# Performance work log

Hardware: AMD Instinct MI355X
Metric: run time of the kernel (lower is better)

The kernel has to match this reference:

```python
import jax, jax.numpy as jnp
import numpy as np

D, H, DH, DFF, K = 512, 8, 64, 2048, 31
B, T = 8, 1024


def _ln(x, g, b):
    m = x.mean(-1, keepdims=True)
    v = ((x - m) ** 2).mean(-1, keepdims=True)
    return (x - m) / jnp.sqrt(v + 1e-5) * g + b


def _silu(x):
    return x * jax.nn.sigmoid(x)


def _pe(t, d):
    i = jnp.arange(t, dtype=jnp.float32)[:, None]
    j = jnp.arange(0, d, 2, dtype=jnp.float32)
    ang = i * (1.0 / (10000.0 ** (j / d)))
    pe = jnp.zeros((t, d), jnp.float32)
    pe = pe.at[:, 0::2].set(jnp.sin(ang))
    pe = pe.at[:, 1::2].set(jnp.cos(ang))
    return pe


def setup_inputs() -> dict:
    key = jax.random.key(0)
    ks = iter(jax.random.split(key, 40))
    s = 0.02
    d = {
        'x': jax.random.normal(next(ks), (B, T, D), jnp.float32),
        # FF module 1
        'ff1_ln_g': jnp.ones((D,), jnp.float32), 'ff1_ln_b': jnp.zeros((D,), jnp.float32),
        'ff1_w1': jax.random.normal(next(ks), (D, DFF), jnp.float32) * s,
        'ff1_b1': jnp.zeros((DFF,), jnp.float32),
        'ff1_w2': jax.random.normal(next(ks), (DFF, D), jnp.float32) * s,
        'ff1_b2': jnp.zeros((D,), jnp.float32),
        # MHSA
        'mha_ln_g': jnp.ones((D,), jnp.float32), 'mha_ln_b': jnp.zeros((D,), jnp.float32),
        'wq': jax.random.normal(next(ks), (H, D, DH), jnp.float32) * s,
        'bq': jnp.zeros((H, DH), jnp.float32),
        'wk': jax.random.normal(next(ks), (H, D, DH), jnp.float32) * s,
        'bk': jnp.zeros((H, DH), jnp.float32),
        'wv': jax.random.normal(next(ks), (H, D, DH), jnp.float32) * s,
        'bv': jnp.zeros((H, DH), jnp.float32),
        'wo': jax.random.normal(next(ks), (D, D), jnp.float32) * s,
        'bo': jnp.zeros((D,), jnp.float32),
        # Conv module
        'cv_ln_g': jnp.ones((D,), jnp.float32), 'cv_ln_b': jnp.zeros((D,), jnp.float32),
        'cv_w1': jax.random.normal(next(ks), (2 * D, D), jnp.float32) * s,
        'cv_b1': jnp.zeros((2 * D,), jnp.float32),
        'cv_wd': jax.random.normal(next(ks), (D, D, K), jnp.float32) * s,
        'cv_bn_g': jnp.ones((D,), jnp.float32), 'cv_bn_b': jnp.zeros((D,), jnp.float32),
        'cv_w2': jax.random.normal(next(ks), (D, D), jnp.float32) * s,
        'cv_b2': jnp.zeros((D,), jnp.float32),
        # FF module 2
        'ff2_ln_g': jnp.ones((D,), jnp.float32), 'ff2_ln_b': jnp.zeros((D,), jnp.float32),
        'ff2_w1': jax.random.normal(next(ks), (D, DFF), jnp.float32) * s,
        'ff2_b1': jnp.zeros((DFF,), jnp.float32),
        'ff2_w2': jax.random.normal(next(ks), (DFF, D), jnp.float32) * s,
        'ff2_b2': jnp.zeros((D,), jnp.float32),
        # final layer norm
        'fin_g': jnp.ones((D,), jnp.float32), 'fin_b': jnp.zeros((D,), jnp.float32),
    }
    return d


def _block(x, p):
    def ffn(x, g, b, w1, b1, w2, b2):
        y = _silu(_ln(x, g, b) @ w1 + b1) @ w2 + b2
        return x + y  # FeedForwardModule internal residual

    # x = x + 0.5 * ff_1(x)
    x = x + 0.5 * ffn(x, p['ff1_ln_g'], p['ff1_ln_b'], p['ff1_w1'], p['ff1_b1'], p['ff1_w2'], p['ff1_b2'])

    # MHSA module (with its own internal residual), then block residual
    y = _ln(x, p['mha_ln_g'], p['mha_ln_b']) + _pe(x.shape[1], x.shape[2])
    q = jnp.einsum('btd,hde->bhte', y, p['wq']) + p['bq'][None, :, None, :]
    k = jnp.einsum('btd,hde->bhte', y, p['wk']) + p['bk'][None, :, None, :]
    v = jnp.einsum('btd,hde->bhte', y, p['wv']) + p['bv'][None, :, None, :]
    scores = jnp.einsum('bhtd,bhsd->bhts', q, k) * (1.0 / np.sqrt(DH))
    attn = jax.nn.softmax(scores, axis=-1)
    o = jnp.einsum('bhts,bhsd->bhtd', attn, v)
    # faithful to original: raw view [B,H,T,dh] -> [B,T,H*dh] (no transpose)
    o = o.reshape(x.shape[0], x.shape[1], H * DH)
    o = o @ p['wo'] + p['bo']
    x = x + (x + o)

    # Convolution module (internal residual), then block residual
    y = _ln(x, p['cv_ln_g'], p['cv_ln_b']).swapaxes(1, 2)  # [B,D,T]
    y = jnp.einsum('ed,bdt->bet', p['cv_w1'], y) + p['cv_b1'][None, :, None]
    a, g = jnp.split(y, 2, axis=1)
    y = a * jax.nn.sigmoid(g)  # GLU over channel dim
    y = jax.lax.conv_general_dilated(y, p['cv_wd'], (1,), [(K // 2, K // 2)],
                                     dimension_numbers=('NCH', 'OIH', 'NCH'))
    # BatchNorm1d in training mode: batch stats over (batch, time), biased variance
    m = y.mean((0, 2), keepdims=True)
    var = ((y - m) ** 2).mean((0, 2), keepdims=True)
    y = (y - m) / jnp.sqrt(var + 1e-5) * p['cv_bn_g'][None, :, None] + p['cv_bn_b'][None, :, None]
    y = _silu(y)
    y = jnp.einsum('ed,bdt->bet', p['cv_w2'], y) + p['cv_b2'][None, :, None]
    y = y.swapaxes(1, 2)
    x = x + (x + y)

    # x = x + 0.5 * ff_2(x)
    x = x + 0.5 * ffn(x, p['ff2_ln_g'], p['ff2_ln_b'], p['ff2_w1'], p['ff2_b1'], p['ff2_w2'], p['ff2_b2'])

    return _ln(x, p['fin_g'], p['fin_b'])


def reference(x, ff1_ln_g, ff1_ln_b, ff1_w1, ff1_b1, ff1_w2, ff1_b2,
              mha_ln_g, mha_ln_b, wq, bq, wk, bk, wv, bv, wo, bo,
              cv_ln_g, cv_ln_b, cv_w1, cv_b1, cv_wd, cv_bn_g, cv_bn_b, cv_w2, cv_b2,
              ff2_ln_g, ff2_ln_b, ff2_w1, ff2_b1, ff2_w2, ff2_b2,
              fin_g, fin_b):
    p = dict(ff1_ln_g=ff1_ln_g, ff1_ln_b=ff1_ln_b, ff1_w1=ff1_w1, ff1_b1=ff1_b1,
             ff1_w2=ff1_w2, ff1_b2=ff1_b2, mha_ln_g=mha_ln_g, mha_ln_b=mha_ln_b,
             wq=wq, bq=bq, wk=wk, bk=bk, wv=wv, bv=bv, wo=wo, bo=bo,
             cv_ln_g=cv_ln_g, cv_ln_b=cv_ln_b, cv_w1=cv_w1, cv_b1=cv_b1, cv_wd=cv_wd,
             cv_bn_g=cv_bn_g, cv_bn_b=cv_bn_b, cv_w2=cv_w2, cv_b2=cv_b2,
             ff2_ln_g=ff2_ln_g, ff2_ln_b=ff2_ln_b, ff2_w1=ff2_w1, ff2_b1=ff2_b1,
             ff2_w2=ff2_w2, ff2_b2=ff2_b2, fin_g=fin_g, fin_b=fin_b)
    return _block(x, p)
```

## Files before the change

kernel.cpp:

```cpp
#include <hip/hip_runtime.h>


typedef __attribute__((ext_vector_type(4))) float f32x4;
typedef __attribute__((ext_vector_type(8))) short short8;
typedef __attribute__((ext_vector_type(4))) short s16x4;

__device__ __forceinline__ float bfs2f(short s) {
  unsigned u = ((unsigned)(unsigned short)s) << 16;
  float f; __builtin_memcpy(&f, &u, 4); return f;
}
__device__ __forceinline__ short f2bfs(float f) {
  unsigned u; __builtin_memcpy(&u, &f, 4);
  u = (u + 0x7FFFu + ((u >> 16) & 1u)) >> 16;
  return (short)u;
}
__device__ __forceinline__ float sigmoidf_(float x) { return 1.f / (1.f + __expf(-x)); }

#define GLOADLDS(gsrc, ldst) \
  __builtin_amdgcn_global_load_lds((__attribute__((address_space(1))) void*)(gsrc), \
                                   (__attribute__((address_space(3))) void*)(ldst), 16, 0, 0)

#define VMCNT_ASM(n) asm volatile("s_waitcnt vmcnt(" #n ")" ::: "memory")
template<int N> __device__ __forceinline__ void vmcnt_wait() {
  if      constexpr (N == 0)  VMCNT_ASM(0);
  else if constexpr (N == 2)  VMCNT_ASM(2);
  else if constexpr (N == 3)  VMCNT_ASM(3);
  else if constexpr (N == 4)  VMCNT_ASM(4);
  else if constexpr (N == 6)  VMCNT_ASM(6);
  else if constexpr (N == 8)  VMCNT_ASM(8);
  else                        VMCNT_ASM(0);
}
#define MEMFENCE asm volatile("" ::: "memory")

enum { EPI_SILU = 0, EPI_F32BIAS = 1, EPI_RES = 2, EPI_QKV = 3, EPI_F32 = 6 };

template<int BM, int BN, int WM, int WN, int EPI>
__global__ __launch_bounds__(256) void gemm_bt(
    const short* __restrict__ A, int lda, long zAh, long zAl,
    const short* __restrict__ BT, int ldbt, long zBh, long zBl,
    int K, int Kdec,
    void* C, int ldc, long zCh, long zCl, int zdiv,
    const float* bias, const float* bias2, const float* bias3,
    const float* resid, float alpha, float beta)
{
  constexpr int FM = BM / (WM * 16), FN = BN / (WN * 16);
  constexpr int AIT = (BM * 4) / 256, BIT = (BN * 4) / 256;
  constexpr int L = AIT + BIT;
  __shared__ short sA[3][BM * 32];
  __shared__ short sB[3][BN * 32];
  const int tid = threadIdx.x;
  const int zmask = (1 << zdiv) - 1;
  const int zhi = (int)(blockIdx.z >> zdiv);
  const int zlo = (int)(blockIdx.z & zmask);
  A  += (long)zhi * zAh + (long)zlo * zAl;
  BT += (long)zhi * zBh + (long)zlo * zBl;
  char* cbase = (char*)C + (long)zhi * zCh + (long)zlo * zCl;
  const int m0 = blockIdx.x * BM, n0 = blockIdx.y * BN;
  const int Keff = K - (zlo == zmask ? Kdec : 0);

  auto stage = [&](int buf, int k0) {
#pragma unroll
    for (int it = 0; it < AIT; ++it) {
      int idx = it * 256 + tid;
      GLOADLDS(A + (long)(m0 + (idx >> 2)) * lda + k0 + (idx & 3) * 8, &sA[buf][idx * 8]);
    }
#pragma unroll
    for (int it = 0; it < BIT; ++it) {
      int idx = it * 256 + tid;
      GLOADLDS(BT + (long)(n0 + (idx >> 2)) * ldbt + k0 + (idx & 3) * 8, &sB[buf][idx * 8]);
    }
  };

  f32x4 acc[FM][FN];
#pragma unroll
  for (int i = 0; i < FM; ++i) {
#pragma unroll
    for (int j = 0; j < FN; ++j) acc[i][j] = (f32x4){0.f, 0.f, 0.f, 0.f};
  }
  const int lane = tid & 63, wid = tid >> 6;
  const int wm = wid / WN, wn = wid % WN;
  const int lr = lane & 15, kg = lane >> 4;
  const int aRow = wm * (BM / WM), bRow = wn * (BN / WN);

  const int nt = Keff >> 5;
  stage(0, 0);
  stage(1, 32);
  vmcnt_wait<L>();
  __builtin_amdgcn_s_barrier();

  int cur = 0, sbuf = 2;
  for (int t = 0; t < nt; ++t) {
    const bool st = (t + 2 < nt);
    if (st) stage(sbuf, (t + 2) * 32);
    short8 af[FM], bfr[FN];
#pragma unroll
    for (int mi = 0; mi < FM; ++mi)
      af[mi] = *(const short8*)&sA[cur][(aRow + mi * 16 + lr) * 32 + kg * 8];
#pragma unroll
    for (int ni = 0; ni < FN; ++ni)
      bfr[ni] = *(const short8*)&sB[cur][(bRow + ni * 16 + lr) * 32 + kg * 8];
#pragma unroll
    for (int mi = 0; mi < FM; ++mi) {
#pragma unroll
      for (int ni = 0; ni < FN; ++ni)
        acc[mi][ni] = __builtin_amdgcn_mfma_f32_16x16x32_bf16(af[mi], bfr[ni], acc[mi][ni], 0, 0, 0);
    }
    if (st) vmcnt_wait<L>(); else vmcnt_wait<0>();
    __builtin_amdgcn_s_barrier();
    cur = (cur == 2) ? 0 : cur + 1;
    sbuf = (sbuf == 2) ? 0 : sbuf + 1;
  }

  const int baseRow = m0 + aRow, baseCol = n0 + bRow;
#pragma unroll
  for (int mi = 0; mi < FM; ++mi) {
#pragma unroll
    for (int ni = 0; ni < FN; ++ni) {
      const int col = baseCol + ni * 16 + lr;
#pragma unroll
      for (int r = 0; r < 4; ++r) {
        const int row = baseRow + mi * 16 + kg * 4 + r;
        float v = acc[mi][ni][r];
        if (EPI == EPI_SILU) {
          v += bias[col];
          v = v * sigmoidf_(v);
          ((short*)cbase)[(long)row * ldc + col] = f2bfs(v);
        } else if (EPI == EPI_F32BIAS) {
          v += bias[col];
          ((float*)cbase)[(long)row * ldc + col] = v;
        } else if (EPI == EPI_RES) {
          v += bias[col];
          float rv = resid[(long)row * ldc + col];
          ((float*)cbase)[(long)row * ldc + col] = alpha * rv + beta * v;
        } else if (EPI == EPI_QKV) {
          if (col < 512)       v = (v + bias[col]) * 0.125f;
          else if (col < 1024) v += bias2[col - 512];
          else                 v += bias3[col - 1024];
          ((short*)cbase)[(long)row * ldc + col] = f2bfs(v);
        } else if (EPI == EPI_F32) {
          ((float*)cbase)[(long)row * ldc + col] = v;
        }
      }
    }
  }
}

__global__ __launch_bounds__(256) void conv_tap(
    const short* __restrict__ glu,
    const short* __restrict__ wdP,
    short* __restrict__ parts)
{
  __shared__ short sA[2][144 * 32];
  const int tid = threadIdx.x;
  const int bid = blockIdx.x;
  const int cc = bid & 7, j = bid >> 3;
  const int y = cc >> 1, kg = cc & 1;
  const int x = j & 7, b = j >> 3;
  const int m0 = x * 128, n0 = y * 128;
  const short* Arow0 = glu + ((long)b * 1056 + m0 + 1 + kg * 16) * 512;
  short* cbase = parts + (long)kg * (8192L * 512) + (long)b * (1024L * 512);

  const int lane = tid & 63, wid = tid >> 6;
  const int wm = wid >> 1, wn = wid & 1;
  const int lr = lane & 15, kgr = lane >> 4;
  const int aRow = wm * 64, bRow = wn * 64;

  const short* Bp = wdP + (long)((n0 + bRow) >> 4) * (512L * 512)
                  + (long)(kg * 256) * 512 + lane * 8;
  const long NSTR = 512L * 512;

  auto stageA = [&](int buf, int ib) {
#pragma unroll
    for (int it = 0; it < 3; ++it) {
      int idx = it * 256 + tid;
      if (idx < 576) {
        GLOADLDS(Arow0 + (long)(idx >> 2) * 512 + ib * 32 + (idx & 3) * 8,
                 &sA[buf][idx * 8]);
      }
    }
  };

  f32x4 acc[4][4];
#pragma unroll
  for (int i = 0; i < 4; ++i) {
#pragma unroll
    for (int jj = 0; jj < 4; ++jj) acc[i][jj] = (f32x4){0.f, 0.f, 0.f, 0.f};
  }
  short8 b0[4], b1[4];

  stageA(0, 0);
  MEMFENCE;
#pragma unroll
  for (int ni = 0; ni < 4; ++ni)
    b0[ni] = *(const short8*)(Bp + ni * NSTR);
  MEMFENCE;
  vmcnt_wait<4>();
  __builtin_amdgcn_s_barrier();

  int cur = 0;
  for (int ib = 0; ib < 16; ++ib) {
    if (ib + 1 < 16) stageA(cur ^ 1, ib + 1);
    MEMFENCE;
#pragma unroll
    for (int kk = 0; kk < 16; ++kk) {
      const long noff = (kk + 1 < 16) ? (long)((kk + 1) * 16 + ib) * 512
                                      : (long)(ib + 1) * 512;
      if ((kk & 1) == 0) {
#pragma unroll
        for (int ni = 0; ni < 4; ++ni)
          b1[ni] = *(const short8*)(Bp + noff + ni * NSTR);
      } else {
#pragma unroll
        for (int ni = 0; ni < 4; ++ni)
          b0[ni] = *(const short8*)(Bp + noff + ni * NSTR);
      }
      short8 af[4];
#pragma unroll
      for (int mi = 0; mi < 4; ++mi)
        af[mi] = *(const short8*)&sA[cur][(kk + aRow + mi * 16 + lr) * 32 + kgr * 8];
      __builtin_amdgcn_s_setprio(1);
      if ((kk & 1) == 0) {
#pragma unroll
        for (int mi = 0; mi < 4; ++mi) {
#pragma unroll
          for (int ni = 0; ni < 4; ++ni)
            acc[mi][ni] = __builtin_amdgcn_mfma_f32_16x16x32_bf16(af[mi], b0[ni], acc[mi][ni], 0, 0, 0);
        }
      } else {
#pragma unroll
        for (int mi = 0; mi < 4; ++mi) {
#pragma unroll
          for (int ni = 0; ni < 4; ++ni)
            acc[mi][ni] = __builtin_amdgcn_mfma_f32_16x16x32_bf16(af[mi], b1[ni], acc[mi][ni], 0, 0, 0);
        }
      }
      __builtin_amdgcn_s_setprio(0);
    }
    vmcnt_wait<4>();
    __builtin_amdgcn_s_barrier();
    cur ^= 1;
  }
  vmcnt_wait<0>();

  const int baseRow = m0 + aRow, baseCol = n0 + bRow;
#pragma unroll
  for (int mi = 0; mi < 4; ++mi) {
#pragma unroll
    for (int ni = 0; ni < 4; ++ni) {
      const int col = baseCol + ni * 16 + lr;
#pragma unroll
      for (int r = 0; r < 4; ++r) {
        const int row = baseRow + mi * 16 + kgr * 4 + r;
        cbase[(long)row * 512 + col] = f2bfs(acc[mi][ni][r]);
      }
    }
  }
}

__global__ __launch_bounds__(256) void flash_attn(
    const short* __restrict__ qkv,
    const short* __restrict__ vt,
    short* __restrict__ out)
{
  __shared__ short sQ[64 * 64];
  __shared__ short sK[64 * 64];
  __shared__ short sV[64 * 64];
  __shared__ short sP[4][16 * 64];
  const int tid = threadIdx.x;
  const int lane = tid & 63, w = tid >> 6;
  const int lr = lane & 15, kg = lane >> 4;
  const int bh = (int)blockIdx.z;
  const int b = bh >> 3, h = bh & 7;
  const int q0 = blockIdx.x * 64;
  const short* qbase = qkv + (long)b * 1024 * 1536 + h * 64;
  const short* kbase = qbase + 512;
  const short* vtb = vt + (long)bh * 65536;

#pragma unroll
  for (int it = 0; it < 2; ++it) {
    int idx = it * 256 + tid;
    int row = idx >> 3, c = (idx & 7) ^ (row & 7);
    GLOADLDS(qbase + (long)(q0 + row) * 1536 + c * 8, &sQ[idx * 8]);
  }
  __syncthreads();
  short8 bq[2];
#pragma unroll
  for (int ks = 0; ks < 2; ++ks)
    bq[ks] = *(const short8*)&sQ[(w * 16 + lr) * 64 + ((ks * 4 + kg) ^ (lr & 7)) * 8];

  f32x4 po[4];
#pragma unroll
  for (int mi = 0; mi < 4; ++mi) po[mi] = (f32x4){0.f, 0.f, 0.f, 0.f};
  float m = -3.0e38f, l = 0.f;

  for (int s0 = 0; s0 < 1024; s0 += 64) {
#pragma unroll
    for (int it = 0; it < 2; ++it) {
      int idx = it * 256 + tid;
      int row = idx >> 3, c = (idx & 7) ^ (row & 7);
      GLOADLDS(kbase + (long)(s0 + row) * 1536 + c * 8, &sK[idx * 8]);
    }
#pragma unroll
    for (int it = 0; it < 2; ++it) {
      int idx = it * 256 + tid;
      int row = idx >> 3, c = (idx & 7) ^ (row & 7);
      GLOADLDS(vtb + (long)row * 1024 + s0 + c * 8, &sV[idx * 8]);
    }
    __syncthreads();

    f32x4 as[4];
#pragma unroll
    for (int mi = 0; mi < 4; ++mi) as[mi] = (f32x4){0.f, 0.f, 0.f, 0.f};
    __builtin_amdgcn_s_setprio(1);
#pragma unroll
    for (int ks = 0; ks < 2; ++ks) {
#pragma unroll
      for (int mi = 0; mi < 4; ++mi) {
        short8 ak = *(const short8*)&sK[(mi * 16 + lr) * 64 + ((ks * 4 + kg) ^ (lr & 7)) * 8];
        as[mi] = __builtin_amdgcn_mfma_f32_16x16x32_bf16(ak, bq[ks], as[mi], 0, 0, 0);
      }
    }
    __builtin_amdgcn_s_setprio(0);

    float rmax = as[0][0];
#pragma unroll
    for (int mi = 0; mi < 4; ++mi) {
#pragma unroll
      for (int r = 0; r < 4; ++r) rmax = fmaxf(rmax, as[mi][r]);
    }
    rmax = fmaxf(rmax, __shfl_xor(rmax, 16));
    rmax = fmaxf(rmax, __shfl_xor(rmax, 32));
    const float mn = fmaxf(m, rmax);
    const float sc = __expf(m - mn);
    float p[4][4];
    float rsum = 0.f;
#pragma unroll
    for (int mi = 0; mi < 4; ++mi) {
#pragma unroll
      for (int r = 0; r < 4; ++r) { p[mi][r] = __expf(as[mi][r] - mn); rsum += p[mi][r]; }
    }
    rsum += __shfl_xor(rsum, 16);
    rsum += __shfl_xor(rsum, 32);
    l = l * sc + rsum;
    m = mn;
#pragma unroll
    for (int mi = 0; mi < 4; ++mi) {
#pragma unroll
      for (int r = 0; r < 4; ++r) po[mi][r] *= sc;
    }
#pragma unroll
    for (int mi = 0; mi < 4; ++mi) {
      s16x4 pk;
#pragma unroll
      for (int r = 0; r < 4; ++r) pk[r] = f2bfs(p[mi][r]);
      *(s16x4*)&sP[w][lr * 64 + ((mi ^ (lr & 3)) * 16 + kg * 4)] = pk;
    }
    __builtin_amdgcn_s_setprio(1);
#pragma unroll
    for (int ks = 0; ks < 2; ++ks) {
      short8 bp = *(const short8*)&sP[w][lr * 64 + (((ks * 2 + (kg >> 1)) ^ (lr & 3)) * 16 + (kg & 1) * 8)];
#pragma unroll
      for (int mi = 0; mi < 4; ++mi) {
        short8 av = *(const short8*)&sV[(mi * 16 + lr) * 64 + ((ks * 4 + kg) ^ (lr & 7)) * 8];
        po[mi] = __builtin_amdgcn_mfma_f32_16x16x32_bf16(av, bp, po[mi], 0, 0, 0);
      }
    }
    __builtin_amdgcn_s_setprio(0);
    __syncthreads();
  }

  const float inv = 1.f / l;
  const int t2 = q0 + w * 16 + lr;
  const int n = h * 1024 + t2;
  short* ob = out + ((long)b * 1024 + (n >> 3)) * 512 + (n & 7) * 64;
#pragma unroll
  for (int mi = 0; mi < 4; ++mi) {
    s16x4 o;
#pragma unroll
    for (int r = 0; r < 4; ++r) o[r] = f2bfs(po[mi][r] * inv);
    *(s16x4*)&ob[mi * 16 + kg * 4] = o;
  }
}

__global__ __launch_bounds__(256) void reduce_bn(
    const short* __restrict__ parts, long pstride,
    short* __restrict__ z, float* stats)
{
  const int r0 = blockIdx.x * 16;
  const int c = threadIdx.x * 2;
  float s0 = 0.f, s1 = 0.f, q0 = 0.f, q1 = 0.f;
#pragma unroll 4
  for (int r = 0; r < 16; ++r) {
    const long idx = (long)(r0 + r) * 512 + c;
    int p0 = *(const int*)&parts[idx];
    int p1 = *(const int*)&parts[idx + pstride];
    float a0 = bfs2f((short)(p0 & 0xffff)) + bfs2f((short)(p1 & 0xffff));
    float a1 = bfs2f((short)(p0 >> 16)) + bfs2f((short)(p1 >> 16));
    int zo = ((int)(unsigned short)f2bfs(a0)) | (((int)(unsigned short)f2bfs(a1)) << 16);
    *(int*)&z[idx] = zo;
    s0 += a0; s1 += a1; q0 += a0 * a0; q1 += a1 * a1;
  }
  atomicAdd(&stats[c], s0);
  atomicAdd(&stats[c + 1], s1);
  atomicAdd(&stats[512 + c], q0);
  atomicAdd(&stats[512 + c + 1], q1);
}

template<int ADDPE, int OUTF32>
__global__ __launch_bounds__(256) void ln_rows(
    const float* __restrict__ X, const float* __restrict__ g, const float* __restrict__ b,
    const float* __restrict__ pe, void* __restrict__ Y)
{
  const int row = blockIdx.x * 4 + (threadIdx.x >> 6);
  const int lane = threadIdx.x & 63;
  const int c0 = lane * 8;
  const float* src = X + (long)row * 512 + c0;
  f32x4 a = *(const f32x4*)src, c = *(const f32x4*)(src + 4);
  float x[8] = {a[0], a[1], a[2], a[3], c[0], c[1], c[2], c[3]};
  float s = 0.f, q = 0.f;
#pragma unroll
  for (int j = 0; j < 8; ++j) { s += x[j]; q += x[j] * x[j]; }
#pragma unroll
  for (int off = 32; off > 0; off >>= 1) { s += __shfl_xor(s, off); q += __shfl_xor(q, off); }
  const float mean = s * (1.f / 512.f);
  const float var = q * (1.f / 512.f) - mean * mean;
  const float rstd = rsqrtf(var + 1e-5f);
  f32x4 g0 = *(const f32x4*)(g + c0), g1 = *(const f32x4*)(g + c0 + 4);
  f32x4 b0 = *(const f32x4*)(b + c0), b1 = *(const f32x4*)(b + c0 + 4);
  float gg[8] = {g0[0], g0[1], g0[2], g0[3], g1[0], g1[1], g1[2], g1[3]};
  float bb[8] = {b0[0], b0[1], b0[2], b0[3], b1[0], b1[1], b1[2], b1[3]};
  float y[8];
#pragma unroll
  for (int j = 0; j < 8; ++j) {
    y[j] = (x[j] - mean) * rstd * gg[j] + bb[j];
    if (ADDPE) y[j] += pe[(long)(row & 1023) * 512 + c0 + j];
  }
  if (OUTF32) {
    float* dst = (float*)Y + (long)row * 512 + c0;
    *(f32x4*)dst = (f32x4){y[0], y[1], y[2], y[3]};
    *(f32x4*)(dst + 4) = (f32x4){y[4], y[5], y[6], y[7]};
  } else {
    short8 o;
#pragma unroll
    for (int j = 0; j < 8; ++j) o[j] = f2bfs(y[j]);
    *(short8*)((short*)Y + (long)row * 512 + c0) = o;
  }
}

template<int INF32>
__global__ __launch_bounds__(256) void transpose64(
    const void* __restrict__ in_, int ldin, short* __restrict__ out, int ldout,
    int ctiles, int zshift, long zh_in, long zl_in, long z_out)
{
  __shared__ short t[64][72];
  const int z = blockIdx.z;
  const long inoff = (long)(z >> zshift) * zh_in + (long)(z & ((1 << zshift) - 1)) * zl_in;
  const int tr = blockIdx.x / ctiles, tc = blockIdx.x % ctiles;
  short* dst = out + (long)z * z_out + (long)(tc * 64) * ldout + tr * 64;
  const int tid = threadIdx.x;
#pragma unroll
  for (int p = 0; p < 2; ++p) {
    int idx = p * 256 + tid;
    int r = idx >> 3, c8 = (idx & 7) * 8;
    if (INF32) {
      const float* src = (const float*)in_ + inoff + (long)(tr * 64 + r) * ldin + tc * 64 + c8;
      f32x4 v0 = *(const f32x4*)src, v1 = *(const f32x4*)(src + 4);
#pragma unroll
      for (int j = 0; j < 4; ++j) { t[r][c8 + j] = f2bfs(v0[j]); t[r][c8 + 4 + j] = f2bfs(v1[j]); }
    } else {
      const short* src = (const short*)in_ + inoff + (long)(tr * 64 + r) * ldin + tc * 64 + c8;
      short8 v = *(const short8*)src;
#pragma unroll
      for (int j = 0; j < 8; ++j) t[r][c8 + j] = v[j];
    }
  }
  __syncthreads();
#pragma unroll
  for (int p = 0; p < 2; ++p) {
    int idx = p * 256 + tid;
    int c = idx >> 3, r8 = (idx & 7) * 8;
    short8 v;
#pragma unroll
    for (int j = 0; j < 8; ++j) v[j] = t[r8 + j][c];
    *(short8*)(dst + (long)c * ldout + r8) = v;
  }
}

__global__ __launch_bounds__(256) void wd_pack(const float* __restrict__ wd, short* __restrict__ wdP)
{
  const int gid = blockIdx.x * 256 + threadIdx.x;
  const int e = gid >> 9, i = gid & 511;
  const float* src = wd + ((long)e * 512 + i) * 31;
  const long rowtile = (long)(e >> 4) * (512L * 512);
  const int inner = ((i >> 3) & 3) * 128 + (e & 15) * 8 + (i & 7);
#pragma unroll
  for (int KK = 0; KK < 31; ++KK)
    wdP[rowtile + (long)(KK * 16 + (i >> 5)) * 512 + inner] = f2bfs(src[KK]);
  wdP[rowtile + (long)(31 * 16 + (i >> 5)) * 512 + inner] = 0;
}

__global__ __launch_bounds__(256) void pe_init(float* __restrict__ pe)
{
  const int gid = blockIdx.x * 256 + threadIdx.x;
  const int t = gid >> 8, p = gid & 255;
  const float freq = __expf(-(float)p * (9.210340371976184f / 256.f));
  const float ang = (float)t * freq;
  pe[(long)t * 512 + 2 * p]     = sinf(ang);
  pe[(long)t * 512 + 2 * p + 1] = cosf(ang);
}

__global__ __launch_bounds__(256) void glu_kernel(const float* __restrict__ y1, short* __restrict__ gp)
{
  const int gid = blockIdx.x * 256 + threadIdx.x;
  const int row = gid >> 7;
  const int ci = (gid & 127) * 4;
  const float* base = y1 + (long)row * 1024;
  f32x4 a = *(const f32x4*)(base + ci);
  f32x4 g = *(const f32x4*)(base + 512 + ci);
  const int b = row >> 10, t = row & 1023;
  s16x4 o;
#pragma unroll
  for (int j = 0; j < 4; ++j) o[j] = f2bfs(a[j] * sigmoidf_(g[j]));
  *(s16x4*)(gp + ((long)b * 1056 + 16 + t) * 512 + ci) = o;
}

__global__ void bn_stats(float* stats, const float* __restrict__ bn_g, const float* __restrict__ bn_b)
{
  const int c = blockIdx.x * 256 + threadIdx.x;
  if (c < 512) {
    float mean = stats[c] * (1.f / 8192.f);
    float var = stats[512 + c] * (1.f / 8192.f) - mean * mean;
    float sc = bn_g[c] * rsqrtf(var + 1e-5f);
    stats[1024 + c] = sc;
    stats[1536 + c] = bn_b[c] - mean * sc;
  }
}

__global__ __launch_bounds__(256) void bn_silu(const short* __restrict__ z, const float* __restrict__ stats,
                                               short* __restrict__ out)
{
  const long base = ((long)blockIdx.x * 256 + threadIdx.x) * 8;
  const int c0 = (int)(base & 511);
  short8 v = *(const short8*)(z + base);
  short8 o;
#pragma unroll
  for (int j = 0; j < 8; ++j) {
    const int c = c0 + j;
    float y = bfs2f(v[j]) * stats[1024 + c] + stats[1536 + c];
    o[j] = f2bfs(y * sigmoidf_(y));
  }
  *(short8*)(out + base) = o;
}

__global__ __launch_bounds__(256) void cast_bf16(const float* __restrict__ in, short* __restrict__ out, long n)
{
  for (long i = (long)blockIdx.x * 256 + threadIdx.x; i < n; i += (long)gridDim.x * 256)
    out[i] = f2bfs(in[i]);
}

extern "C" void kernel_launch(void* const* d_in, const int* in_sizes, int n_in,
                              void* d_out, int out_size, void* d_ws, size_t ws_size,
                              hipStream_t stream)
{
  (void)in_sizes; (void)n_in; (void)out_size; (void)ws_size;
  const float* x_in   = (const float*)d_in[0];
  const float* ff1_g  = (const float*)d_in[1];
  const float* ff1_bb = (const float*)d_in[2];
  const float* ff1_w1 = (const float*)d_in[3];
  const float* ff1_b1 = (const float*)d_in[4];
  const float* ff1_w2 = (const float*)d_in[5];
  const float* ff1_b2 = (const float*)d_in[6];
  const float* mha_g  = (const float*)d_in[7];
  const float* mha_b  = (const float*)d_in[8];
  const float* wq     = (const float*)d_in[9];
  const float* bq     = (const float*)d_in[10];
  const float* wk     = (const float*)d_in[11];
  const float* bk     = (const float*)d_in[12];
  const float* wv     = (const float*)d_in[13];
  const float* bv     = (const float*)d_in[14];
  const float* wo     = (const float*)d_in[15];
  const float* bo     = (const float*)d_in[16];
  const float* cv_g   = (const float*)d_in[17];
  const float* cv_b   = (const float*)d_in[18];
  const float* cv_w1  = (const float*)d_in[19];
  const float* cv_b1  = (const float*)d_in[20];
  const float* cv_wd  = (const float*)d_in[21];
  const float* bn_g   = (const float*)d_in[22];
  const float* bn_b   = (const float*)d_in[23];
  const float* cv_w2  = (const float*)d_in[24];
  const float* cv_b2  = (const float*)d_in[25];
  const float* ff2_g  = (const float*)d_in[26];
  const float* ff2_b  = (const float*)d_in[27];
  const float* ff2_w1 = (const float*)d_in[28];
  const float* ff2_b1 = (const float*)d_in[29];
  const float* ff2_w2 = (const float*)d_in[30];
  const float* ff2_b2 = (const float*)d_in[31];
  const float* fin_g  = (const float*)d_in[32];
  const float* fin_b  = (const float*)d_in[33];

  size_t off = 0;
  char* wsb = (char*)d_ws;
  auto take = [&](size_t n) { char* p = wsb + off; off += (n + 255) & ~(size_t)255; return p; };
  short* ff1w1T = (short*)take(2048L * 512 * 2);
  short* ff1w2T = (short*)take(512L * 2048 * 2);
  short* qkvT   = (short*)take(1536L * 512 * 2);
  short* woT    = (short*)take(512L * 512 * 2);
  short* cw1b   = (short*)take(1024L * 512 * 2);
  short* cw2b   = (short*)take(512L * 512 * 2);
  short* wdP    = (short*)take(32L * 512 * 512 * 2);
  short* ff2w1T = (short*)take(2048L * 512 * 2);
  short* ff2w2T = (short*)take(512L * 2048 * 2);
  float* xcur   = (float*)take(8192L * 512 * 4);
  char*  Ra     = take(8192L * 2048 * 2);
  short* Rb     = (short*)take(8192L * 512 * 2);
  short* Rg     = (short*)take((8L * 1056 + 2) * 512 * 2);
  short* parts  = (short*)take(2L * 8192 * 512 * 2);
  short* vt     = (short*)take(64L * 64 * 1024 * 2);
  float* pe     = (float*)take(1024L * 512 * 4);
  float* stats  = (float*)take(2048L * 4);

  short* hid = (short*)Ra;
  short* qkv = (short*)Ra;
  float* y1  = (float*)Ra;

  transpose64<1><<<dim3(256, 1, 1), 256, 0, stream>>>(ff1_w1, 2048, ff1w1T, 512, 32, 0, 0, 0, 0);
  transpose64<1><<<dim3(256, 1, 1), 256, 0, stream>>>(ff1_w2, 512, ff1w2T, 2048, 8, 0, 0, 0, 0);
  transpose64<1><<<dim3(8, 1, 8), 256, 0, stream>>>(wq, 64, qkvT, 512, 1, 0, 32768, 0, 32768);
  transpose64<1><<<dim3(8, 1, 8), 256, 0, stream>>>(wk, 64, qkvT + 512 * 512, 512, 1, 0, 32768, 0, 32768);
  transpose64<1><<<dim3(8, 1, 8), 256, 0, stream>>>(wv, 64, qkvT + 1024 * 512, 512, 1, 0, 32768, 0, 32768);
  transpose64<1><<<dim3(64, 1, 1), 256, 0, stream>>>(wo, 512, woT, 512, 8, 0, 0, 0, 0);
  transpose64<1><<<dim3(256, 1, 1), 256, 0, stream>>>(ff2_w1, 2048, ff2w1T, 512, 32, 0, 0, 0, 0);
  transpose64<1><<<dim3(256, 1, 1), 256, 0, stream>>>(ff2_w2, 512, ff2w2T, 2048, 8, 0, 0, 0, 0);
  wd_pack<<<1024, 256, 0, stream>>>(cv_wd, wdP);
  pe_init<<<1024, 256, 0, stream>>>(pe);
  cast_bf16<<<2048, 256, 0, stream>>>(cv_w1, cw1b, 524288L);
  cast_bf16<<<1024, 256, 0, stream>>>(cv_w2, cw2b, 262144L);

  ln_rows<0, 0><<<2048, 256, 0, stream>>>(x_in, ff1_g, ff1_bb, nullptr, Rb);
  gemm_bt<128, 128, 2, 2, EPI_SILU><<<dim3(64, 16, 1), 256, 0, stream>>>(
      Rb, 512, 0, 0, ff1w1T, 512, 0, 0, 512, 0,
      hid, 2048, 0, 0, 0, ff1_b1, nullptr, nullptr, nullptr, 0.f, 0.f);
  gemm_bt<64, 64, 2, 2, EPI_RES><<<dim3(128, 8, 1), 256, 0, stream>>>(
      hid, 2048, 0, 0, ff1w2T, 2048, 0, 0, 2048, 0,
      xcur, 512, 0, 0, 0, ff1_b2, nullptr, nullptr, x_in, 1.5f, 0.5f);

  ln_rows<1, 0><<<2048, 256, 0, stream>>>(xcur, mha_g, mha_b, pe, Rb);
  gemm_bt<128, 128, 2, 2, EPI_QKV><<<dim3(64, 12, 1), 256, 0, stream>>>(
      Rb, 512, 0, 0, qkvT, 512, 0, 0, 512, 0,
      qkv, 1536, 0, 0, 0, bq, bk, bv, nullptr, 0.f, 0.f);
  transpose64<0><<<dim3(16, 1, 64), 256, 0, stream>>>(qkv + 1024, 1536, vt, 1024, 1, 3,
                                                      1024L * 1536, 64, 65536);
  flash_attn<<<dim3(16, 1, 64), 256, 0, stream>>>(qkv, vt, Rb);
  gemm_bt<64, 64, 2, 2, EPI_RES><<<dim3(128, 8, 1), 256, 0, stream>>>(
      Rb, 512, 0, 0, woT, 512, 0, 0, 512, 0,
      xcur, 512, 0, 0, 0, bo, nullptr, nullptr, xcur, 2.f, 1.f);

  ln_rows<0, 0><<<2048, 256, 0, stream>>>(xcur, cv_g, cv_b, nullptr, Rb);
  gemm_bt<128, 128, 2, 2, EPI_F32BIAS><<<dim3(64, 8, 1), 256, 0, stream>>>(
      Rb, 512, 0, 0, cw1b, 512, 0, 0, 512, 0,
      y1, 1024, 0, 0, 0, cv_b1, nullptr, nullptr, nullptr, 0.f, 0.f);
  (void)hipMemsetAsync(Rg, 0, (8L * 1056 + 2) * 512 * 2, stream);
  glu_kernel<<<4096, 256, 0, stream>>>(y1, Rg);
  (void)hipMemsetAsync(stats, 0, 1024 * sizeof(float), stream);
  conv_tap<<<512, 256, 0, stream>>>(Rg, wdP, parts);
  reduce_bn<<<512, 256, 0, stream>>>(parts, 8192L * 512, Rb, stats);
  bn_stats<<<2, 256, 0, stream>>>(stats, bn_g, bn_b);
  bn_silu<<<2048, 256, 0, stream>>>(Rb, stats, (short*)Rg);
  gemm_bt<64, 64, 2, 2, EPI_RES><<<dim3(128, 8, 1), 256, 0, stream>>>(
      (short*)Rg, 512, 0, 0, cw2b, 512, 0, 0, 512, 0,
      xcur, 512, 0, 0, 0, cv_b2, nullptr, nullptr, xcur, 2.f, 1.f);

  ln_rows<0, 0><<<2048, 256, 0, stream>>>(xcur, ff2_g, ff2_b, nullptr, Rb);
  gemm_bt<128, 128, 2, 2, EPI_SILU><<<dim3(64, 16, 1), 256, 0, stream>>>(
      Rb, 512, 0, 0, ff2w1T, 512, 0, 0, 512, 0,
      hid, 2048, 0, 0, 0, ff2_b1, nullptr, nullptr, nullptr, 0.f, 0.f);
  gemm_bt<64, 64, 2, 2, EPI_RES><<<dim3(128, 8, 1), 256, 0, stream>>>(
      hid, 2048, 0, 0, ff2w2T, 2048, 0, 0, 2048, 0,
      xcur, 512, 0, 0, 0, ff2_b2, nullptr, nullptr, xcur, 1.5f, 0.5f);

  ln_rows<0, 1><<<2048, 256, 0, stream>>>(xcur, fin_g, fin_b, nullptr, (float*)d_out);
}
```

Measured before the change: 508.0 us.

## Store conv pointwise output in bf16, zero only halo rows, raise MFMA priority

The first conv pointwise GEMM now writes bf16 instead of fp32, which halves the y1 write and the GLU read traffic, and the GLU kernel converts on load. The full memset of the padded GLU buffer is replaced by a small kernel that zeroes only the halo rows the GLU kernel does not write. The GEMM main loop also wraps its MFMA block in s_setprio 1/0 so these waves get scheduling priority. The extra bf16 rounding of the pre-GLU activations adds a small accuracy risk.

```diff
diff --git a/kernel.cpp b/kernel.cpp
--- a/kernel.cpp
+++ b/kernel.cpp
@@ -32,7 +32,7 @@
 }
 #define MEMFENCE asm volatile("" ::: "memory")
 
-enum { EPI_SILU = 0, EPI_F32BIAS = 1, EPI_RES = 2, EPI_QKV = 3, EPI_F32 = 6 };
+enum { EPI_SILU = 0, EPI_BBIAS = 1, EPI_RES = 2, EPI_QKV = 3, EPI_F32 = 6 };
 
 template<int BM, int BN, int WM, int WN, int EPI>
 __global__ __launch_bounds__(256) void gemm_bt(
@@ -99,12 +99,14 @@
 #pragma unroll
     for (int ni = 0; ni < FN; ++ni)
       bfr[ni] = *(const short8*)&sB[cur][(bRow + ni * 16 + lr) * 32 + kg * 8];
+    __builtin_amdgcn_s_setprio(1);
 #pragma unroll
     for (int mi = 0; mi < FM; ++mi) {
 #pragma unroll
       for (int ni = 0; ni < FN; ++ni)
         acc[mi][ni] = __builtin_amdgcn_mfma_f32_16x16x32_bf16(af[mi], bfr[ni], acc[mi][ni], 0, 0, 0);
     }
+    __builtin_amdgcn_s_setprio(0);
     if (st) vmcnt_wait<L>(); else vmcnt_wait<0>();
     __builtin_amdgcn_s_barrier();
     cur = (cur == 2) ? 0 : cur + 1;
@@ -125,9 +127,9 @@
           v += bias[col];
           v = v * sigmoidf_(v);
           ((short*)cbase)[(long)row * ldc + col] = f2bfs(v);
-        } else if (EPI == EPI_F32BIAS) {
+        } else if (EPI == EPI_BBIAS) {
           v += bias[col];
-          ((float*)cbase)[(long)row * ldc + col] = v;
+          ((short*)cbase)[(long)row * ldc + col] = f2bfs(v);
         } else if (EPI == EPI_RES) {
           v += bias[col];
           float rv = resid[(long)row * ldc + col];
@@ -509,18 +511,37 @@
   pe[(long)t * 512 + 2 * p + 1] = cosf(ang);
 }
 
-__global__ __launch_bounds__(256) void glu_kernel(const float* __restrict__ y1, short* __restrict__ gp)
+__global__ __launch_bounds__(256) void halo_zero(short* __restrict__ gp)
+{
+  const int gid = blockIdx.x * 256 + threadIdx.x;
+  if (gid >= 16512) return;
+  long row;
+  int c8;
+  if (gid < 16384) {
+    const int b = gid >> 11;
+    const int r = (gid >> 6) & 31;
+    c8 = (gid & 63) * 8;
+    row = (long)b * 1056 + ((r < 16) ? r : (1024 + r));
+  } else {
+    const int k = gid - 16384;
+    c8 = (k & 63) * 8;
+    row = 8448 + (k >> 6);
+  }
+  *(short8*)(gp + row * 512 + c8) = (short8){0, 0, 0, 0, 0, 0, 0, 0};
+}
+
+__global__ __launch_bounds__(256) void glu_kernel(const short* __restrict__ y1, short* __restrict__ gp)
 {
   const int gid = blockIdx.x * 256 + threadIdx.x;
   const int row = gid >> 7;
   const int ci = (gid & 127) * 4;
-  const float* base = y1 + (long)row * 1024;
-  f32x4 a = *(const f32x4*)(base + ci);
-  f32x4 g = *(const f32x4*)(base + 512 + ci);
+  const short* base = y1 + (long)row * 1024;
+  s16x4 a = *(const s16x4*)(base + ci);
+  s16x4 g = *(const s16x4*)(base + 512 + ci);
   const int b = row >> 10, t = row & 1023;
   s16x4 o;
 #pragma unroll
-  for (int j = 0; j < 4; ++j) o[j] = f2bfs(a[j] * sigmoidf_(g[j]));
+  for (int j = 0; j < 4; ++j) o[j] = f2bfs(bfs2f(a[j]) * sigmoidf_(bfs2f(g[j])));
   *(s16x4*)(gp + ((long)b * 1056 + 16 + t) * 512 + ci) = o;
 }
 
@@ -621,7 +642,7 @@
 
   short* hid = (short*)Ra;
   short* qkv = (short*)Ra;
-  float* y1  = (float*)Ra;
+  short* y1  = (short*)Ra;
 
   transpose64<1><<<dim3(256, 1, 1), 256, 0, stream>>>(ff1_w1, 2048, ff1w1T, 512, 32, 0, 0, 0, 0);
   transpose64<1><<<dim3(256, 1, 1), 256, 0, stream>>>(ff1_w2, 512, ff1w2T, 2048, 8, 0, 0, 0, 0);
@@ -656,10 +677,10 @@
       xcur, 512, 0, 0, 0, bo, nullptr, nullptr, xcur, 2.f, 1.f);
 
   ln_rows<0, 0><<<2048, 256, 0, stream>>>(xcur, cv_g, cv_b, nullptr, Rb);
-  gemm_bt<128, 128, 2, 2, EPI_F32BIAS><<<dim3(64, 8, 1), 256, 0, stream>>>(
+  gemm_bt<128, 128, 2, 2, EPI_BBIAS><<<dim3(64, 8, 1), 256, 0, stream>>>(
       Rb, 512, 0, 0, cw1b, 512, 0, 0, 512, 0,
       y1, 1024, 0, 0, 0, cv_b1, nullptr, nullptr, nullptr, 0.f, 0.f);
-  (void)hipMemsetAsync(Rg, 0, (8L * 1056 + 2) * 512 * 2, stream);
+  halo_zero<<<65, 256, 0, stream>>>(Rg);
   glu_kernel<<<4096, 256, 0, stream>>>(y1, Rg);
   (void)hipMemsetAsync(stats, 0, 1024 * sizeof(float), stream);
   conv_tap<<<512, 256, 0, stream>>>(Rg, wdP, parts);
```

Result: no change. 498.2 us (-1.9%).
